# Kernel optimization log

Hardware: AMD Instinct MI355X
Metric: run time of the kernel (lower is better)

## Reference

```python
import jax, jax.numpy as jnp
import numpy as np

NEG_INF = jnp.float32(-1e30)


def setup_inputs() -> dict:
    key = jax.random.key(0)
    ks = jax.random.split(key, 7)
    B, Lx, Lm, d = 4, 256, 256, 256
    return {
        "x": jax.random.normal(ks[0], (B, Lx, d), dtype=jnp.float32),
        "memory": jax.random.normal(ks[1], (B, Lm, d), dtype=jnp.float32),
        "memory_mask": jax.random.randint(ks[2], (B, Lm), 0, 2, dtype=jnp.int32),
        "ws1_w": jax.random.normal(ks[3], (d, d), dtype=jnp.float32) * 0.05,
        "ws1_b": jax.random.normal(ks[4], (d,), dtype=jnp.float32) * 0.05,
        "ws2_w": jax.random.normal(ks[5], (d, d), dtype=jnp.float32) * 0.05,
        "wst_w": jax.random.normal(ks[6], (1, d), dtype=jnp.float32) * 0.05,
    }


def reference(x, memory, memory_mask, ws1_w, ws1_b, ws2_w, wst_w):
    # x: [B, Lx, d], memory: [B, Lm, d]; torch Linear: y = x @ W.T + b
    item1 = jnp.einsum('bxd,ed->bxe', x, ws1_w) + ws1_b          # [B, Lx, d]
    item2 = jnp.einsum('bmd,ed->bme', memory, ws2_w)             # [B, Lm, d]
    item = jnp.tanh(item1[:, :, None, :] + item2[:, None, :, :])  # [B, Lx, Lm, d]
    S = jnp.einsum('bxmd,d->bxm', item, wst_w[0])                # [B, Lx, Lm]
    # agg_2_h uses the UNMASKED scores, softmax over Lx after transpose
    agg_2_h = jnp.einsum('bmx,bxd->bmd', jax.nn.softmax(S.transpose(0, 2, 1), axis=-1), x)
    # mask applied to S before the main attention readout
    S = jnp.where(memory_mask[:, None, :] == 0, NEG_INF, S)      # [B, Lx, Lm]
    out = jnp.einsum('bxm,bmd->bxd', jax.nn.softmax(S, axis=-1), memory)
    return (out, S, agg_2_h)
```

## Files before the change

### kernel.cpp

```cpp
#include <hip/hip_runtime.h>

static constexpr int NB = 4;
static constexpr int L  = 256;
static constexpr int D  = 256;

__device__ __forceinline__ float fast_rcp(float x) {
#if __has_builtin(__builtin_amdgcn_rcpf)
    return __builtin_amdgcn_rcpf(x);
#else
    return 1.0f / x;
#endif
}

__device__ __forceinline__ float fast_exp(float x) {
#if __has_builtin(__builtin_amdgcn_exp2f)
    return __builtin_amdgcn_exp2f(x * 1.4426950408889634f);
#else
    return __expf(x);
#endif
}

__device__ __forceinline__ float exp_2x(float x) {
#if __has_builtin(__builtin_amdgcn_exp2f)
    return __builtin_amdgcn_exp2f(x * 2.8853900817779268f);
#else
    return __expf(2.0f * x);
#endif
}

__global__ __launch_bounds__(256) void linear_kernel(
    const float* __restrict__ x, const float* __restrict__ mem,
    const float* __restrict__ w1, const float* __restrict__ b1,
    const float* __restrict__ w2,
    float* __restrict__ E1X, float* __restrict__ E2X,
    float* __restrict__ E1R, float* __restrict__ E2R)
{
    const int bid = blockIdx.x;
    const int rb  = (bid >> 3) * 32;
    const int cb  = (bid & 7) * 32;
    const int which = rb >= 1024;
    const int rloc  = which ? rb - 1024 : rb;
    const float* src = which ? mem : x;
    const float* W   = which ? w2  : w1;
    float* dstX = which ? E2X : E1X;
    float* dstR = which ? E2R : E1R;

    constexpr int P4 = 65;
    __shared__ __align__(16) float4 xs4[32 * P4];
    __shared__ __align__(16) float4 ws4[32 * P4];

    const int t = threadIdx.x;
    const float4* src4 = reinterpret_cast<const float4*>(src) + rloc * 64;
    const float4* Wg4  = reinterpret_cast<const float4*>(W)   + cb   * 64;
#pragma unroll
    for (int k = 0; k < 8; ++k) {
        int idx = k * 256 + t;
        int r = idx >> 6, c = idx & 63;
        xs4[r * P4 + c] = src4[r * 64 + c];
        ws4[r * P4 + c] = Wg4[r * 64 + c];
    }
    __syncthreads();

    const int rr = t >> 4, cc = t & 15;
    const float4* a0p = xs4 + rr * P4;
    const float4* a1p = xs4 + (rr + 16) * P4;
    const float4* w0p = ws4 + cc * P4;
    const float4* w1p = ws4 + (cc + 16) * P4;
    float acc00 = 0.f, acc01 = 0.f, acc10 = 0.f, acc11 = 0.f;
#pragma unroll 4
    for (int d4 = 0; d4 < 64; ++d4) {
        float4 a0 = a0p[d4], a1 = a1p[d4];
        float4 w0 = w0p[d4], w1 = w1p[d4];
        acc00 = fmaf(a0.x, w0.x, acc00); acc00 = fmaf(a0.y, w0.y, acc00);
        acc00 = fmaf(a0.z, w0.z, acc00); acc00 = fmaf(a0.w, w0.w, acc00);
        acc01 = fmaf(a0.x, w1.x, acc01); acc01 = fmaf(a0.y, w1.y, acc01);
        acc01 = fmaf(a0.z, w1.z, acc01); acc01 = fmaf(a0.w, w1.w, acc01);
        acc10 = fmaf(a1.x, w0.x, acc10); acc10 = fmaf(a1.y, w0.y, acc10);
        acc10 = fmaf(a1.z, w0.z, acc10); acc10 = fmaf(a1.w, w0.w, acc10);
        acc11 = fmaf(a1.x, w1.x, acc11); acc11 = fmaf(a1.y, w1.y, acc11);
        acc11 = fmaf(a1.z, w1.z, acc11); acc11 = fmaf(a1.w, w1.w, acc11);
    }
    const float bias0 = which ? 0.f : b1[cb + cc];
    const float bias1 = which ? 0.f : b1[cb + cc + 16];
    const float e00 = exp_2x(acc00 + bias0);
    const float e01 = exp_2x(acc01 + bias1);
    const float e10 = exp_2x(acc10 + bias0);
    const float e11 = exp_2x(acc11 + bias1);
    const int c0 = cb + cc, c1 = cb + cc + 16;
    const int rA = rloc + rr, rB = rloc + rr + 16;
    dstX[((c0 >> 2) * 1024 + rA) * 4 + (c0 & 3)] = e00;
    dstX[((c1 >> 2) * 1024 + rA) * 4 + (c1 & 3)] = e01;
    dstX[((c0 >> 2) * 1024 + rB) * 4 + (c0 & 3)] = e10;
    dstX[((c1 >> 2) * 1024 + rB) * 4 + (c1 & 3)] = e11;
    dstR[rA * D + c0] = e00;
    dstR[rA * D + c1] = e01;
    dstR[rB * D + c0] = e10;
    dstR[rB * D + c1] = e11;
}

__global__ __launch_bounds__(256) void fused2_kernel(
    const float* __restrict__ x, const float* __restrict__ mem,
    const int* __restrict__ mask, const float* __restrict__ wst,
    const float* __restrict__ E1X, const float* __restrict__ E2X,
    const float* __restrict__ E1R, const float* __restrict__ E2R,
    float* __restrict__ out, float* __restrict__ Smask, float* __restrict__ agg)
{
    int bid = blockIdx.x;
    const bool isRow = bid < 256;
    if (!isRow) bid -= 256;
    const int b    = bid >> 6;
    const int r0   = (bid & 63) * 4;
    const int base = b * L;
    const int t    = threadIdx.x;
    const int w    = t >> 6, l = t & 63;

    const float4* laneE  = reinterpret_cast<const float4*>(isRow ? E2X : E1X);
    const float4* stripR = reinterpret_cast<const float4*>(isRow ? E1R : E2R);

    __shared__ __align__(16) float4 sstrip[4][64];
    __shared__ __align__(16) float4 swst[64];
    __shared__ __align__(16) float  sS[4][L];
    __shared__ __align__(16) float4 part[4][4][64];

    {
        int j = t >> 6, c = t & 63;
        sstrip[j][c] = stripR[(base + r0 + j) * 64 + c];
        if (t < 64) swst[t] = reinterpret_cast<const float4*>(wst)[t];
    }
    __syncthreads();

    float W_tot;
    {
        float4 wv = swst[l];
        float s = (wv.x + wv.y) + (wv.z + wv.w);
#pragma unroll
        for (int o = 32; o; o >>= 1) s += __shfl_xor(s, o);
        W_tot = s;
    }

    float acc0 = 0.f, acc1 = 0.f, acc2 = 0.f, acc3 = 0.f;
#pragma unroll 4
    for (int d4 = 0; d4 < 64; ++d4) {
        float4 ev = laneE[d4 * 1024 + base + t];
        float4 s0 = sstrip[0][d4];
        float4 s1 = sstrip[1][d4];
        float4 s2 = sstrip[2][d4];
        float4 s3 = sstrip[3][d4];
        float4 wv = swst[d4];
        acc0 = fmaf(wv.x, fast_rcp(fmaf(ev.x, s0.x, 1.f)), acc0);
        acc0 = fmaf(wv.y, fast_rcp(fmaf(ev.y, s0.y, 1.f)), acc0);
        acc0 = fmaf(wv.z, fast_rcp(fmaf(ev.z, s0.z, 1.f)), acc0);
        acc0 = fmaf(wv.w, fast_rcp(fmaf(ev.w, s0.w, 1.f)), acc0);
        acc1 = fmaf(wv.x, fast_rcp(fmaf(ev.x, s1.x, 1.f)), acc1);
        acc1 = fmaf(wv.y, fast_rcp(fmaf(ev.y, s1.y, 1.f)), acc1);
        acc1 = fmaf(wv.z, fast_rcp(fmaf(ev.z, s1.z, 1.f)), acc1);
        acc1 = fmaf(wv.w, fast_rcp(fmaf(ev.w, s1.w, 1.f)), acc1);
        acc2 = fmaf(wv.x, fast_rcp(fmaf(ev.x, s2.x, 1.f)), acc2);
        acc2 = fmaf(wv.y, fast_rcp(fmaf(ev.y, s2.y, 1.f)), acc2);
        acc2 = fmaf(wv.z, fast_rcp(fmaf(ev.z, s2.z, 1.f)), acc2);
        acc2 = fmaf(wv.w, fast_rcp(fmaf(ev.w, s2.w, 1.f)), acc2);
        acc3 = fmaf(wv.x, fast_rcp(fmaf(ev.x, s3.x, 1.f)), acc3);
        acc3 = fmaf(wv.y, fast_rcp(fmaf(ev.y, s3.y, 1.f)), acc3);
        acc3 = fmaf(wv.z, fast_rcp(fmaf(ev.z, s3.z, 1.f)), acc3);
        acc3 = fmaf(wv.w, fast_rcp(fmaf(ev.w, s3.w, 1.f)), acc3);
    }
    float S0 = fmaf(-2.f, acc0, W_tot);
    float S1 = fmaf(-2.f, acc1, W_tot);
    float S2 = fmaf(-2.f, acc2, W_tot);
    float S3 = fmaf(-2.f, acc3, W_tot);

    if (isRow) {
        const bool dead = (mask[base + t] == 0);
        Smask[((base + r0 + 0) << 8) + t] = dead ? -1e30f : S0;
        Smask[((base + r0 + 1) << 8) + t] = dead ? -1e30f : S1;
        Smask[((base + r0 + 2) << 8) + t] = dead ? -1e30f : S2;
        Smask[((base + r0 + 3) << 8) + t] = dead ? -1e30f : S3;
        sS[0][t] = dead ? 0.f : fast_exp(S0);
        sS[1][t] = dead ? 0.f : fast_exp(S1);
        sS[2][t] = dead ? 0.f : fast_exp(S2);
        sS[3][t] = dead ? 0.f : fast_exp(S3);
    } else {
        sS[0][t] = fast_exp(S0);
        sS[1][t] = fast_exp(S1);
        sS[2][t] = fast_exp(S2);
        sS[3][t] = fast_exp(S3);
    }
    __syncthreads();

    float rs_w;
    {
        float4 ev4 = reinterpret_cast<const float4*>(sS[w])[l];
        float s = (ev4.x + ev4.y) + (ev4.z + ev4.w);
#pragma unroll
        for (int o = 32; o; o >>= 1) s += __shfl_xor(s, o);
        rs_w = fast_rcp(s);
    }

    const float4* V4 = reinterpret_cast<const float4*>(isRow ? mem : x) + base * 64;
    float4 acc[4];
#pragma unroll
    for (int r = 0; r < 4; ++r) acc[r] = make_float4(0.f, 0.f, 0.f, 0.f);

#pragma unroll 2
    for (int k4 = 0; k4 < 16; ++k4) {
        const int m0 = w * 64 + k4 * 4;
        float4 v0 = V4[(m0 + 0) * 64 + l];
        float4 v1 = V4[(m0 + 1) * 64 + l];
        float4 v2 = V4[(m0 + 2) * 64 + l];
        float4 v3 = V4[(m0 + 3) * 64 + l];
#pragma unroll
        for (int r = 0; r < 4; ++r) {
            float4 pr = *reinterpret_cast<const float4*>(&sS[r][m0]);
            acc[r].x = fmaf(pr.x, v0.x, acc[r].x); acc[r].y = fmaf(pr.x, v0.y, acc[r].y);
            acc[r].z = fmaf(pr.x, v0.z, acc[r].z); acc[r].w = fmaf(pr.x, v0.w, acc[r].w);
            acc[r].x = fmaf(pr.y, v1.x, acc[r].x); acc[r].y = fmaf(pr.y, v1.y, acc[r].y);
            acc[r].z = fmaf(pr.y, v1.z, acc[r].z); acc[r].w = fmaf(pr.y, v1.w, acc[r].w);
            acc[r].x = fmaf(pr.z, v2.x, acc[r].x); acc[r].y = fmaf(pr.z, v2.y, acc[r].y);
            acc[r].z = fmaf(pr.z, v2.z, acc[r].z); acc[r].w = fmaf(pr.z, v2.w, acc[r].w);
            acc[r].x = fmaf(pr.w, v3.x, acc[r].x); acc[r].y = fmaf(pr.w, v3.y, acc[r].y);
            acc[r].z = fmaf(pr.w, v3.z, acc[r].z); acc[r].w = fmaf(pr.w, v3.w, acc[r].w);
        }
    }
#pragma unroll
    for (int r = 0; r < 4; ++r) part[r][w][l] = acc[r];
    __syncthreads();

    {
        float4 q0 = part[w][0][l], q1 = part[w][1][l];
        float4 q2 = part[w][2][l], q3 = part[w][3][l];
        float4 ov;
        ov.x = ((q0.x + q1.x) + (q2.x + q3.x)) * rs_w;
        ov.y = ((q0.y + q1.y) + (q2.y + q3.y)) * rs_w;
        ov.z = ((q0.z + q1.z) + (q2.z + q3.z)) * rs_w;
        ov.w = ((q0.w + q1.w) + (q2.w + q3.w)) * rs_w;
        float* o = isRow ? out : agg;
        reinterpret_cast<float4*>(o)[((base + r0 + w) << 6) + l] = ov;
    }
}

extern "C" void kernel_launch(void* const* d_in, const int* in_sizes, int n_in,
                              void* d_out, int out_size, void* d_ws, size_t ws_size,
                              hipStream_t stream)
{
    const float* x    = (const float*)d_in[0];
    const float* mem  = (const float*)d_in[1];
    const int*   mask = (const int*)  d_in[2];
    const float* w1   = (const float*)d_in[3];
    const float* b1   = (const float*)d_in[4];
    const float* w2   = (const float*)d_in[5];
    const float* wst  = (const float*)d_in[6];

    float* out   = (float*)d_out;
    float* Smask = out + NB * L * L;
    float* agg   = Smask + NB * L * L;

    float* E1X = (float*)d_ws;
    float* E2X = E1X + NB * L * D;
    float* E1R = E2X + NB * L * D;
    float* E2R = E1R + NB * L * D;

    linear_kernel<<<512, 256, 0, stream>>>(x, mem, w1, b1, w2, E1X, E2X, E1R, E2R);
    fused2_kernel<<<512, 256, 0, stream>>>(x, mem, mask, wst, E1X, E2X, E1R, E2R,
                                           out, Smask, agg);
}
```

Measured before the change: 41.70 us.

## Process eight rows per block and interleave batches across blocks

Each block of the fused scoring kernel now handles 8 rows instead of 4. This halves the grid to 256 blocks and doubles reuse of each laneE load and each V load across rows. The block-to-work mapping also changes so consecutive blocks cycle through batch and side. The trade-off is more registers and LDS per block and fewer blocks, which may leave part of the 256-CU device underused or lower occupancy.

```diff
diff --git a/kernel.cpp b/kernel.cpp
--- a/kernel.cpp
+++ b/kernel.cpp
@@ -105,26 +105,29 @@
     const float* __restrict__ E1R, const float* __restrict__ E2R,
     float* __restrict__ out, float* __restrict__ Smask, float* __restrict__ agg)
 {
-    int bid = blockIdx.x;
-    const bool isRow = bid < 256;
-    if (!isRow) bid -= 256;
-    const int b    = bid >> 6;
-    const int r0   = (bid & 63) * 4;
+    const int bid  = blockIdx.x;
+    const int p    = bid & 7, g = bid >> 3;
+    const int side = p >> 2,  b = p & 3;
     const int base = b * L;
+    const int r0   = g * 8;
     const int t    = threadIdx.x;
     const int w    = t >> 6, l = t & 63;
 
-    const float4* laneE  = reinterpret_cast<const float4*>(isRow ? E2X : E1X);
-    const float4* stripR = reinterpret_cast<const float4*>(isRow ? E1R : E2R);
-
-    __shared__ __align__(16) float4 sstrip[4][64];
+    const float4* laneE  = reinterpret_cast<const float4*>(side ? E1X : E2X);
+    const float4* stripR = reinterpret_cast<const float4*>(side ? E2R : E1R);
+
+    __shared__ __align__(16) float4 sstrip[8][64];
     __shared__ __align__(16) float4 swst[64];
-    __shared__ __align__(16) float  sS[4][L];
-    __shared__ __align__(16) float4 part[4][4][64];
+    __shared__ __align__(16) float  sS[8][L];
+    __shared__ __align__(16) float4 part[8][4][64];
 
     {
-        int j = t >> 6, c = t & 63;
-        sstrip[j][c] = stripR[(base + r0 + j) * 64 + c];
+#pragma unroll
+        for (int k = 0; k < 2; ++k) {
+            int idx = k * 256 + t;
+            int j = idx >> 6, c = idx & 63;
+            sstrip[j][c] = stripR[(base + r0 + j) * 64 + c];
+        }
         if (t < 64) swst[t] = reinterpret_cast<const float4*>(wst)[t];
     }
     __syncthreads();
@@ -139,67 +142,54 @@
     }
 
     float acc0 = 0.f, acc1 = 0.f, acc2 = 0.f, acc3 = 0.f;
-#pragma unroll 4
+    float acc4 = 0.f, acc5 = 0.f, acc6 = 0.f, acc7 = 0.f;
+#pragma unroll 2
     for (int d4 = 0; d4 < 64; ++d4) {
         float4 ev = laneE[d4 * 1024 + base + t];
-        float4 s0 = sstrip[0][d4];
-        float4 s1 = sstrip[1][d4];
-        float4 s2 = sstrip[2][d4];
-        float4 s3 = sstrip[3][d4];
         float4 wv = swst[d4];
-        acc0 = fmaf(wv.x, fast_rcp(fmaf(ev.x, s0.x, 1.f)), acc0);
-        acc0 = fmaf(wv.y, fast_rcp(fmaf(ev.y, s0.y, 1.f)), acc0);
-        acc0 = fmaf(wv.z, fast_rcp(fmaf(ev.z, s0.z, 1.f)), acc0);
-        acc0 = fmaf(wv.w, fast_rcp(fmaf(ev.w, s0.w, 1.f)), acc0);
-        acc1 = fmaf(wv.x, fast_rcp(fmaf(ev.x, s1.x, 1.f)), acc1);
-        acc1 = fmaf(wv.y, fast_rcp(fmaf(ev.y, s1.y, 1.f)), acc1);
-        acc1 = fmaf(wv.z, fast_rcp(fmaf(ev.z, s1.z, 1.f)), acc1);
-        acc1 = fmaf(wv.w, fast_rcp(fmaf(ev.w, s1.w, 1.f)), acc1);
-        acc2 = fmaf(wv.x, fast_rcp(fmaf(ev.x, s2.x, 1.f)), acc2);
-        acc2 = fmaf(wv.y, fast_rcp(fmaf(ev.y, s2.y, 1.f)), acc2);
-        acc2 = fmaf(wv.z, fast_rcp(fmaf(ev.z, s2.z, 1.f)), acc2);
-        acc2 = fmaf(wv.w, fast_rcp(fmaf(ev.w, s2.w, 1.f)), acc2);
-        acc3 = fmaf(wv.x, fast_rcp(fmaf(ev.x, s3.x, 1.f)), acc3);
-        acc3 = fmaf(wv.y, fast_rcp(fmaf(ev.y, s3.y, 1.f)), acc3);
-        acc3 = fmaf(wv.z, fast_rcp(fmaf(ev.z, s3.z, 1.f)), acc3);
-        acc3 = fmaf(wv.w, fast_rcp(fmaf(ev.w, s3.w, 1.f)), acc3);
-    }
-    float S0 = fmaf(-2.f, acc0, W_tot);
-    float S1 = fmaf(-2.f, acc1, W_tot);
-    float S2 = fmaf(-2.f, acc2, W_tot);
-    float S3 = fmaf(-2.f, acc3, W_tot);
-
-    if (isRow) {
+#define TERM(J, ACC)                                                   \
+        {   float4 sv = sstrip[J][d4];                                 \
+            ACC = fmaf(wv.x, fast_rcp(fmaf(ev.x, sv.x, 1.f)), ACC);    \
+            ACC = fmaf(wv.y, fast_rcp(fmaf(ev.y, sv.y, 1.f)), ACC);    \
+            ACC = fmaf(wv.z, fast_rcp(fmaf(ev.z, sv.z, 1.f)), ACC);    \
+            ACC = fmaf(wv.w, fast_rcp(fmaf(ev.w, sv.w, 1.f)), ACC); }
+        TERM(0, acc0) TERM(1, acc1) TERM(2, acc2) TERM(3, acc3)
+        TERM(4, acc4) TERM(5, acc5) TERM(6, acc6) TERM(7, acc7)
+#undef TERM
+    }
+    float S[8];
+    S[0] = fmaf(-2.f, acc0, W_tot); S[1] = fmaf(-2.f, acc1, W_tot);
+    S[2] = fmaf(-2.f, acc2, W_tot); S[3] = fmaf(-2.f, acc3, W_tot);
+    S[4] = fmaf(-2.f, acc4, W_tot); S[5] = fmaf(-2.f, acc5, W_tot);
+    S[6] = fmaf(-2.f, acc6, W_tot); S[7] = fmaf(-2.f, acc7, W_tot);
+
+    if (side == 0) {
         const bool dead = (mask[base + t] == 0);
-        Smask[((base + r0 + 0) << 8) + t] = dead ? -1e30f : S0;
-        Smask[((base + r0 + 1) << 8) + t] = dead ? -1e30f : S1;
-        Smask[((base + r0 + 2) << 8) + t] = dead ? -1e30f : S2;
-        Smask[((base + r0 + 3) << 8) + t] = dead ? -1e30f : S3;
-        sS[0][t] = dead ? 0.f : fast_exp(S0);
-        sS[1][t] = dead ? 0.f : fast_exp(S1);
-        sS[2][t] = dead ? 0.f : fast_exp(S2);
-        sS[3][t] = dead ? 0.f : fast_exp(S3);
+#pragma unroll
+        for (int j = 0; j < 8; ++j) {
+            Smask[((base + r0 + j) << 8) + t] = dead ? -1e30f : S[j];
+            sS[j][t] = dead ? 0.f : fast_exp(S[j]);
+        }
     } else {
-        sS[0][t] = fast_exp(S0);
-        sS[1][t] = fast_exp(S1);
-        sS[2][t] = fast_exp(S2);
-        sS[3][t] = fast_exp(S3);
-    }
-    __syncthreads();
-
-    float rs_w;
-    {
-        float4 ev4 = reinterpret_cast<const float4*>(sS[w])[l];
-        float s = (ev4.x + ev4.y) + (ev4.z + ev4.w);
+#pragma unroll
+        for (int j = 0; j < 8; ++j) sS[j][t] = fast_exp(S[j]);
+    }
+    __syncthreads();
+
+    float rs0, rs1;
+#pragma unroll
+    for (int rr = w, it = 0; rr < 8; rr += 4, ++it) {
+        float4 e4 = reinterpret_cast<const float4*>(sS[rr])[l];
+        float s = (e4.x + e4.y) + (e4.z + e4.w);
 #pragma unroll
         for (int o = 32; o; o >>= 1) s += __shfl_xor(s, o);
-        rs_w = fast_rcp(s);
-    }
-
-    const float4* V4 = reinterpret_cast<const float4*>(isRow ? mem : x) + base * 64;
-    float4 acc[4];
-#pragma unroll
-    for (int r = 0; r < 4; ++r) acc[r] = make_float4(0.f, 0.f, 0.f, 0.f);
+        if (it == 0) rs0 = fast_rcp(s); else rs1 = fast_rcp(s);
+    }
+
+    const float4* V4 = reinterpret_cast<const float4*>(side ? x : mem) + base * 64;
+    float4 acc[8];
+#pragma unroll
+    for (int r = 0; r < 8; ++r) acc[r] = make_float4(0.f, 0.f, 0.f, 0.f);
 
 #pragma unroll 2
     for (int k4 = 0; k4 < 16; ++k4) {
@@ -209,7 +199,7 @@
         float4 v2 = V4[(m0 + 2) * 64 + l];
         float4 v3 = V4[(m0 + 3) * 64 + l];
 #pragma unroll
-        for (int r = 0; r < 4; ++r) {
+        for (int r = 0; r < 8; ++r) {
             float4 pr = *reinterpret_cast<const float4*>(&sS[r][m0]);
             acc[r].x = fmaf(pr.x, v0.x, acc[r].x); acc[r].y = fmaf(pr.x, v0.y, acc[r].y);
             acc[r].z = fmaf(pr.x, v0.z, acc[r].z); acc[r].w = fmaf(pr.x, v0.w, acc[r].w);
@@ -222,19 +212,21 @@
         }
     }
 #pragma unroll
-    for (int r = 0; r < 4; ++r) part[r][w][l] = acc[r];
-    __syncthreads();
-
-    {
-        float4 q0 = part[w][0][l], q1 = part[w][1][l];
-        float4 q2 = part[w][2][l], q3 = part[w][3][l];
+    for (int r = 0; r < 8; ++r) part[r][w][l] = acc[r];
+    __syncthreads();
+
+    float* o = side ? agg : out;
+#pragma unroll
+    for (int rr = w, it = 0; rr < 8; rr += 4, ++it) {
+        float rs = (it == 0) ? rs0 : rs1;
+        float4 q0 = part[rr][0][l], q1 = part[rr][1][l];
+        float4 q2 = part[rr][2][l], q3 = part[rr][3][l];
         float4 ov;
-        ov.x = ((q0.x + q1.x) + (q2.x + q3.x)) * rs_w;
-        ov.y = ((q0.y + q1.y) + (q2.y + q3.y)) * rs_w;
-        ov.z = ((q0.z + q1.z) + (q2.z + q3.z)) * rs_w;
-        ov.w = ((q0.w + q1.w) + (q2.w + q3.w)) * rs_w;
-        float* o = isRow ? out : agg;
-        reinterpret_cast<float4*>(o)[((base + r0 + w) << 6) + l] = ov;
+        ov.x = ((q0.x + q1.x) + (q2.x + q3.x)) * rs;
+        ov.y = ((q0.y + q1.y) + (q2.y + q3.y)) * rs;
+        ov.z = ((q0.z + q1.z) + (q2.z + q3.z)) * rs;
+        ov.w = ((q0.w + q1.w) + (q2.w + q3.w)) * rs;
+        reinterpret_cast<float4*>(o)[((base + r0 + rr) << 6) + l] = ov;
     }
 }
 
@@ -260,6 +252,6 @@
     float* E2R = E1R + NB * L * D;
 
     linear_kernel<<<512, 256, 0, stream>>>(x, mem, w1, b1, w2, E1X, E2X, E1R, E2R);
-    fused2_kernel<<<512, 256, 0, stream>>>(x, mem, mask, wst, E1X, E2X, E1R, E2R,
+    fused2_kernel<<<256, 256, 0, stream>>>(x, mem, mask, wst, E1X, E2X, E1R, E2R,
                                            out, Smask, agg);
 }
```

Result: slower. 43.12 us (+3.4%).
